# Kernel tuning notes

Hardware: AMD Instinct MI355X
Metric: run time of the kernel (lower is better)

## Reference

```python
import jax, jax.numpy as jnp
import numpy as np

B, NNODE, FIN, FOUT = 64, 512, 64, 64

def setup_inputs() -> dict:
    key = jax.random.key(0)
    ks = jax.random.split(key, 8)
    stdW = 1.0 / np.sqrt(FIN)
    stdA = 1.0 / np.sqrt(FOUT)
    return {
        "X": jax.random.normal(ks[0], (B, NNODE, FIN), dtype=jnp.float32),
        "A": jax.random.uniform(ks[1], (B, NNODE, NNODE), dtype=jnp.float32),
        "N": jax.random.randint(ks[2], (B,), 1, NNODE + 1, dtype=jnp.int64),
        "W": jax.random.uniform(ks[3], (FIN, FOUT), jnp.float32, -stdW, stdW),
        "a": jax.random.uniform(ks[4], (FOUT, FOUT), jnp.float32, -stdA, stdA),
        "bias_W": jax.random.uniform(ks[5], (FOUT,), jnp.float32, -stdW, stdW),
        "bias_a": jax.random.uniform(ks[6], (NNODE,), jnp.float32, -1.0 / np.sqrt(NNODE), 1.0 / np.sqrt(NNODE)),
    }

def reference(X, A, N, W, a, bias_W, bias_a):
    # A_ = A + identity on the top-left n_atoms block (only diagonal entries)
    idx = jnp.arange(A.shape[1])
    diag_mask = (idx[None, :] < N[:, None]).astype(A.dtype)  # [B, n]
    A_ = A + jnp.einsum('bn,nm->bnm', diag_mask, jnp.eye(A.shape[1], dtype=A.dtype))
    # XW: [B, n, F_out]
    XW = jnp.einsum('bnc,cd->bnd', X, W)
    # buf[a,j,k] = sum_i a[i,j] * XW^T[a,j,k]  (einsum 'ij,ajk->ajk')
    col_sum = a.sum(axis=0)  # [F_out]
    XWT = jnp.swapaxes(XW, 1, 2)  # [B, F_out, n]
    buf = col_sum[None, :, None] * XWT
    Z = jnp.einsum('bif,bfk->bik', XW, buf) + bias_a  # [B, n, n] + [n] broadcast on last dim
    att = jnp.tanh(jnp.einsum('bij,bjk->bik', A_, Z))
    H = jnp.einsum('bij,bjd->bid', att, XW) + bias_W
    return H
```

## Files before the change

### kernel.cpp

```cpp
#include <hip/hip_runtime.h>

#define BB 64
#define NN 512
#define FD 64

typedef short bf16x8 __attribute__((ext_vector_type(8)));
typedef float f32x4 __attribute__((ext_vector_type(4)));

__device__ __forceinline__ unsigned short f2bf(float f){
    unsigned u = __builtin_bit_cast(unsigned, f);
    u += 0x7fffu + ((u >> 16) & 1u);
    return (unsigned short)(u >> 16);
}
__device__ __forceinline__ float bf2f(unsigned short h){
    unsigned u = ((unsigned)h) << 16;
    return __builtin_bit_cast(float, u);
}
__device__ __forceinline__ float fast_tanh(float x){
    float e = __expf(2.0f * x);
    return 1.0f - 2.0f * __builtin_amdgcn_rcpf(e + 1.0f);
}
__device__ __forceinline__ bf16x8 pack8(float4 a, float4 b){
    bf16x8 r;
    r[0]=(short)f2bf(a.x); r[1]=(short)f2bf(a.y); r[2]=(short)f2bf(a.z); r[3]=(short)f2bf(a.w);
    r[4]=(short)f2bf(b.x); r[5]=(short)f2bf(b.y); r[6]=(short)f2bf(b.z); r[7]=(short)f2bf(b.w);
    return r;
}

__global__ __launch_bounds__(256) void k_prep(const float* __restrict__ W,
                                              const float* __restrict__ a,
                                              float* __restrict__ colsum,
                                              unsigned short* __restrict__ Wt){
    __shared__ float Wl[64][68];
    __shared__ float cpart[4][64];
    int t = threadIdx.x;
    int d = t & 63, part = t >> 6;
    float s = 0.f;
    #pragma unroll
    for (int i = 0; i < 16; i++) s += a[(part*16 + i)*64 + d];
    cpart[part][d] = s;
    int r = t >> 2, c0 = (t & 3) * 16;
    {
        const float4* src = (const float4*)&W[r*64 + c0];
        #pragma unroll
        for (int q = 0; q < 4; q++) *(float4*)&Wl[r][c0 + q*4] = src[q];
    }
    __syncthreads();
    if (part == 0) colsum[d] = cpart[0][d] + cpart[1][d] + cpart[2][d] + cpart[3][d];
    #pragma unroll
    for (int q = 0; q < 4; q++){
        ushort4 o;
        #pragma unroll
        for (int jj = 0; jj < 4; jj++)
            ((unsigned short*)&o)[jj] = f2bf(Wl[c0 + q*4 + jj][r]);
        *(ushort4*)&Wt[r*64 + c0 + q*4] = o;
    }
}

#define XWH_BYTE(n, f)  ((unsigned)(n)*128u + (((((unsigned)(f) >> 3) ^ ((unsigned)(n) & 7u)) & 7u) << 4) + (((unsigned)(f) & 7u) << 1))
#define XWH_B128(n, f0) ((unsigned)(n)*128u + (((((unsigned)(f0) >> 3) ^ ((unsigned)(n) & 7u)) & 7u) << 4))

__global__ __launch_bounds__(512, 1) void k_fused(const float* __restrict__ X,
                                               const float* __restrict__ A,
                                               const unsigned short* __restrict__ Wt,
                                               const float* __restrict__ colsum,
                                               const int* __restrict__ Ni,
                                               const float* __restrict__ bias_a,
                                               const float* __restrict__ bias_W,
                                               float* __restrict__ H){
    __shared__ unsigned short XWtL[64][520];
    __shared__ unsigned short XWhL[512*64];
    __shared__ unsigned short Pl[8][16][72];
    __shared__ unsigned short Wtl[64][72];
    __shared__ float bl[512];
    __shared__ float csl[64];
    int t = threadIdx.x;
    int b = blockIdx.x, it2 = blockIdx.y;
    int lane = t & 63, w = t >> 6, l15 = lane & 15, quad = lane >> 4;
    int tl = w >> 2, st = w & 3;
    int i0 = (it2 + 4*tl) * 64;
    int Nb = (Ni[1] == 0) ? Ni[2*b] : Ni[b];
    const float* Xb = X + (size_t)b*NN*FD;
    const float* Arow = A + (size_t)(b*NN + i0 + st*16 + l15)*NN + quad*8;

    float4 xv[8][2];
    #pragma unroll
    for (int rt = 0; rt < 4; rt++)
        #pragma unroll
        for (int ks = 0; ks < 2; ks++){
            const float* p = &Xb[(w*64 + rt*16 + l15)*FD + ks*32 + quad*8];
            xv[rt*2 + ks][0] = *(const float4*)p;
            xv[rt*2 + ks][1] = *(const float4*)(p + 4);
        }
    float4 pa[4][2];
    #pragma unroll
    for (int s = 0; s < 4; s++){
        pa[s][0] = *(const float4*)&Arow[s*32];
        pa[s][1] = *(const float4*)&Arow[s*32 + 4];
    }
    *(uint4*)&Wtl[t >> 3][(t & 7)*8] = *(const uint4*)&Wt[(t >> 3)*64 + (t & 7)*8];
    bl[t] = bias_a[t];
    if (t < 64) csl[t] = colsum[t];
    __syncthreads();

    #pragma unroll
    for (int rt = 0; rt < 4; rt++){
        f32x4 c[4] = {{0,0,0,0},{0,0,0,0},{0,0,0,0},{0,0,0,0}};
        #pragma unroll
        for (int ks = 0; ks < 2; ks++){
            bf16x8 af = pack8(xv[rt*2 + ks][0], xv[rt*2 + ks][1]);
            #pragma unroll
            for (int nt = 0; nt < 4; nt++){
                bf16x8 bfr = *(const bf16x8*)&Wtl[nt*16 + l15][ks*32 + quad*8];
                c[nt] = __builtin_amdgcn_mfma_f32_16x16x32_bf16(af, bfr, c[nt], 0, 0, 0);
            }
        }
        #pragma unroll
        for (int nt = 0; nt < 4; nt++)
            #pragma unroll
            for (int rg = 0; rg < 4; rg++){
                unsigned short hb = f2bf(c[nt][rg]);
                int n = w*64 + rt*16 + quad*4 + rg, f = nt*16 + l15;
                *(unsigned short*)((char*)XWhL + XWH_BYTE(n, f)) = hb;
                XWtL[f][n] = hb;
            }
    }
    __syncthreads();

    f32x4 acc[4] = {{0,0,0,0},{0,0,0,0},{0,0,0,0},{0,0,0,0}};
    float rs = 0.f;
    #pragma unroll
    for (int s = 0; s < 16; s++){
        float4 v0 = pa[s & 3][0], v1 = pa[s & 3][1];
        if (s < 12){
            pa[s & 3][0] = *(const float4*)&Arow[(s + 4)*32];
            pa[s & 3][1] = *(const float4*)&Arow[(s + 4)*32 + 4];
        }
        rs += (v0.x + v0.y) + (v0.z + v0.w) + (v1.x + v1.y) + (v1.z + v1.w);
        bf16x8 af = pack8(v0, v1);
        #pragma unroll
        for (int nt = 0; nt < 4; nt++){
            bf16x8 bfr = *(const bf16x8*)&XWtL[nt*16 + l15][s*32 + quad*8];
            acc[nt] = __builtin_amdgcn_mfma_f32_16x16x32_bf16(af, bfr, acc[nt], 0, 0, 0);
        }
    }
    #pragma unroll
    for (int nt = 0; nt < 4; nt++)
        #pragma unroll
        for (int rg = 0; rg < 4; rg++){
            int i = i0 + st*16 + quad*4 + rg;
            if (i < Nb)
                acc[nt][rg] += bf2f(*(const unsigned short*)((const char*)XWhL + XWH_BYTE(i, nt*16 + l15)));
        }
    float rsum = rs;
    rsum += __shfl_xor(rsum, 16);
    rsum += __shfl_xor(rsum, 32);
    #pragma unroll
    for (int nt = 0; nt < 4; nt++){
        float cs = csl[nt*16 + l15];
        #pragma unroll
        for (int rg = 0; rg < 4; rg++)
            Pl[w][quad*4 + rg][nt*16 + l15] = f2bf(acc[nt][rg] * cs);
    }
    asm volatile("s_waitcnt lgkmcnt(0)" ::: "memory");
    __builtin_amdgcn_sched_barrier(0);
    bf16x8 maf[2];
    maf[0] = *(const bf16x8*)&Pl[w][l15][quad*8];
    maf[1] = *(const bf16x8*)&Pl[w][l15][32 + quad*8];
    float rs_r[4];
    #pragma unroll
    for (int rg = 0; rg < 4; rg++){
        int i = i0 + st*16 + quad*4 + rg;
        rs_r[rg] = __shfl(rsum, quad*4 + rg) + ((i < Nb) ? 1.f : 0.f);
    }

    f32x4 hacc[4] = {{0,0,0,0},{0,0,0,0},{0,0,0,0},{0,0,0,0}};
    #pragma unroll
    for (int jt = 0; jt < 8; jt++){
        #pragma unroll
        for (int nt = 0; nt < 4; nt++){
            int j = jt*64 + nt*16 + l15;
            float bv = bl[j];
            f32x4 arg = { rs_r[0]*bv, rs_r[1]*bv, rs_r[2]*bv, rs_r[3]*bv };
            #pragma unroll
            for (int ks = 0; ks < 2; ks++){
                bf16x8 bfr = *(const bf16x8*)((const char*)XWhL + XWH_B128(j, ks*32 + quad*8));
                arg = __builtin_amdgcn_mfma_f32_16x16x32_bf16(maf[ks], bfr, arg, 0, 0, 0);
            }
            #pragma unroll
            for (int rg = 0; rg < 4; rg++)
                Pl[w][quad*4 + rg][nt*16 + l15] = f2bf(fast_tanh(arg[rg]));
        }
        asm volatile("s_waitcnt lgkmcnt(0)" ::: "memory");
        __builtin_amdgcn_sched_barrier(0);
        #pragma unroll
        for (int ks = 0; ks < 2; ks++){
            bf16x8 paf = *(const bf16x8*)&Pl[w][l15][ks*32 + quad*8];
            #pragma unroll
            for (int dt = 0; dt < 4; dt++){
                bf16x8 bfr = *(const bf16x8*)&XWtL[dt*16 + l15][jt*64 + ks*32 + quad*8];
                hacc[dt] = __builtin_amdgcn_mfma_f32_16x16x32_bf16(paf, bfr, hacc[dt], 0, 0, 0);
            }
        }
    }
    #pragma unroll
    for (int dt = 0; dt < 4; dt++){
        float bw = bias_W[dt*16 + l15];
        #pragma unroll
        for (int rg = 0; rg < 4; rg++)
            H[(size_t)(b*NN + i0 + st*16 + quad*4 + rg)*FD + dt*16 + l15] = hacc[dt][rg] + bw;
    }
}

extern "C" void kernel_launch(void* const* d_in, const int* in_sizes, int n_in,
                              void* d_out, int out_size, void* d_ws, size_t ws_size,
                              hipStream_t stream){
    const float* X      = (const float*)d_in[0];
    const float* A      = (const float*)d_in[1];
    const int*   N      = (const int*)  d_in[2];
    const float* W      = (const float*)d_in[3];
    const float* a      = (const float*)d_in[4];
    const float* bias_W = (const float*)d_in[5];
    const float* bias_a = (const float*)d_in[6];
    float* H = (float*)d_out;
    char* ws = (char*)d_ws;

    unsigned short* Wt     = (unsigned short*)(ws);
    float*          colsum = (float*)(ws + 8192);

    k_prep <<<1, 256, 0, stream>>>(W, a, colsum, Wt);
    k_fused<<<dim3(BB, 4), 512, 0, stream>>>(X, A, Wt, colsum, N, bias_a, bias_W, H);
}
```

Measured before the change: 126.9 us.

## Swap MFMA operand order to produce transposed tiles and vectorize LDS/global stores

Swaps the A/B operands of the MFMA calls so that each lane's accumulator holds four consecutive columns of one row. This turns scalar 16-bit LDS stores and scalar output writes into packed uint2 and float4 stores. XW is computed twice, once normally and once transposed, and written into padded LDS arrays instead of the swizzled layout. W fragments now live in registers instead of LDS, and the A prefetch depth is doubled from 4 to 8 stages. The change trades extra MFMAs and register pressure for fewer LDS store instructions, fewer shuffles and wider global stores.

```diff
diff --git a/kernel.cpp b/kernel.cpp
--- a/kernel.cpp
+++ b/kernel.cpp
@@ -15,6 +15,9 @@
 __device__ __forceinline__ float bf2f(unsigned short h){
     unsigned u = ((unsigned)h) << 16;
     return __builtin_bit_cast(float, u);
+}
+__device__ __forceinline__ unsigned pkbf2(float a, float b){
+    return (unsigned)f2bf(a) | ((unsigned)f2bf(b) << 16);
 }
 __device__ __forceinline__ float fast_tanh(float x){
     float e = __expf(2.0f * x);
@@ -57,9 +60,6 @@
     }
 }
 
-#define XWH_BYTE(n, f)  ((unsigned)(n)*128u + (((((unsigned)(f) >> 3) ^ ((unsigned)(n) & 7u)) & 7u) << 4) + (((unsigned)(f) & 7u) << 1))
-#define XWH_B128(n, f0) ((unsigned)(n)*128u + (((((unsigned)(f0) >> 3) ^ ((unsigned)(n) & 7u)) & 7u) << 4))
-
 __global__ __launch_bounds__(512, 1) void k_fused(const float* __restrict__ X,
                                                const float* __restrict__ A,
                                                const unsigned short* __restrict__ Wt,
@@ -69,9 +69,8 @@
                                                const float* __restrict__ bias_W,
                                                float* __restrict__ H){
     __shared__ unsigned short XWtL[64][520];
-    __shared__ unsigned short XWhL[512*64];
+    __shared__ unsigned short XWhL[512][72];
     __shared__ unsigned short Pl[8][16][72];
-    __shared__ unsigned short Wtl[64][72];
     __shared__ float bl[512];
     __shared__ float csl[64];
     int t = threadIdx.x;
@@ -92,123 +91,125 @@
             xv[rt*2 + ks][0] = *(const float4*)p;
             xv[rt*2 + ks][1] = *(const float4*)(p + 4);
         }
-    float4 pa[4][2];
-    #pragma unroll
-    for (int s = 0; s < 4; s++){
+    bf16x8 wf[4][2];
+    #pragma unroll
+    for (int ft = 0; ft < 4; ft++)
+        #pragma unroll
+        for (int ks = 0; ks < 2; ks++)
+            wf[ft][ks] = *(const bf16x8*)&Wt[(ft*16 + l15)*64 + ks*32 + quad*8];
+    bl[t] = bias_a[t];
+    if (t < 64) csl[t] = colsum[t];
+
+    #pragma unroll
+    for (int rt = 0; rt < 4; rt++){
+        bf16x8 af0 = pack8(xv[rt*2][0],     xv[rt*2][1]);
+        bf16x8 af1 = pack8(xv[rt*2 + 1][0], xv[rt*2 + 1][1]);
+        f32x4 c[4]  = {{0,0,0,0},{0,0,0,0},{0,0,0,0},{0,0,0,0}};
+        f32x4 ct[4] = {{0,0,0,0},{0,0,0,0},{0,0,0,0},{0,0,0,0}};
+        #pragma unroll
+        for (int nt = 0; nt < 4; nt++){
+            c[nt]  = __builtin_amdgcn_mfma_f32_16x16x32_bf16(af0, wf[nt][0], c[nt], 0, 0, 0);
+            c[nt]  = __builtin_amdgcn_mfma_f32_16x16x32_bf16(af1, wf[nt][1], c[nt], 0, 0, 0);
+            ct[nt] = __builtin_amdgcn_mfma_f32_16x16x32_bf16(wf[nt][0], af0, ct[nt], 0, 0, 0);
+            ct[nt] = __builtin_amdgcn_mfma_f32_16x16x32_bf16(wf[nt][1], af1, ct[nt], 0, 0, 0);
+        }
+        int n0 = w*64 + rt*16;
+        #pragma unroll
+        for (int nt = 0; nt < 4; nt++){
+            uint2 pk = { pkbf2(c[nt][0], c[nt][1]), pkbf2(c[nt][2], c[nt][3]) };
+            *(uint2*)&XWtL[nt*16 + l15][n0 + quad*4] = pk;
+        }
+        #pragma unroll
+        for (int ft = 0; ft < 4; ft++){
+            uint2 pk = { pkbf2(ct[ft][0], ct[ft][1]), pkbf2(ct[ft][2], ct[ft][3]) };
+            *(uint2*)&XWhL[n0 + l15][ft*16 + quad*4] = pk;
+        }
+    }
+    float4 pa[8][2];
+    #pragma unroll
+    for (int s = 0; s < 8; s++){
         pa[s][0] = *(const float4*)&Arow[s*32];
         pa[s][1] = *(const float4*)&Arow[s*32 + 4];
     }
-    *(uint4*)&Wtl[t >> 3][(t & 7)*8] = *(const uint4*)&Wt[(t >> 3)*64 + (t & 7)*8];
-    bl[t] = bias_a[t];
-    if (t < 64) csl[t] = colsum[t];
-    __syncthreads();
-
-    #pragma unroll
-    for (int rt = 0; rt < 4; rt++){
-        f32x4 c[4] = {{0,0,0,0},{0,0,0,0},{0,0,0,0},{0,0,0,0}};
-        #pragma unroll
-        for (int ks = 0; ks < 2; ks++){
-            bf16x8 af = pack8(xv[rt*2 + ks][0], xv[rt*2 + ks][1]);
-            #pragma unroll
-            for (int nt = 0; nt < 4; nt++){
-                bf16x8 bfr = *(const bf16x8*)&Wtl[nt*16 + l15][ks*32 + quad*8];
-                c[nt] = __builtin_amdgcn_mfma_f32_16x16x32_bf16(af, bfr, c[nt], 0, 0, 0);
-            }
-        }
-        #pragma unroll
-        for (int nt = 0; nt < 4; nt++)
-            #pragma unroll
-            for (int rg = 0; rg < 4; rg++){
-                unsigned short hb = f2bf(c[nt][rg]);
-                int n = w*64 + rt*16 + quad*4 + rg, f = nt*16 + l15;
-                *(unsigned short*)((char*)XWhL + XWH_BYTE(n, f)) = hb;
-                XWtL[f][n] = hb;
-            }
-    }
     __syncthreads();
 
     f32x4 acc[4] = {{0,0,0,0},{0,0,0,0},{0,0,0,0},{0,0,0,0}};
     float rs = 0.f;
     #pragma unroll
     for (int s = 0; s < 16; s++){
-        float4 v0 = pa[s & 3][0], v1 = pa[s & 3][1];
-        if (s < 12){
-            pa[s & 3][0] = *(const float4*)&Arow[(s + 4)*32];
-            pa[s & 3][1] = *(const float4*)&Arow[(s + 4)*32 + 4];
+        float4 v0 = pa[s & 7][0], v1 = pa[s & 7][1];
+        if (s < 8){
+            pa[s & 7][0] = *(const float4*)&Arow[(s + 8)*32];
+            pa[s & 7][1] = *(const float4*)&Arow[(s + 8)*32 + 4];
         }
         rs += (v0.x + v0.y) + (v0.z + v0.w) + (v1.x + v1.y) + (v1.z + v1.w);
         bf16x8 af = pack8(v0, v1);
         #pragma unroll
         for (int nt = 0; nt < 4; nt++){
-            bf16x8 bfr = *(const bf16x8*)&XWtL[nt*16 + l15][s*32 + quad*8];
-            acc[nt] = __builtin_amdgcn_mfma_f32_16x16x32_bf16(af, bfr, acc[nt], 0, 0, 0);
-        }
-    }
-    #pragma unroll
-    for (int nt = 0; nt < 4; nt++)
-        #pragma unroll
-        for (int rg = 0; rg < 4; rg++){
-            int i = i0 + st*16 + quad*4 + rg;
-            if (i < Nb)
-                acc[nt][rg] += bf2f(*(const unsigned short*)((const char*)XWhL + XWH_BYTE(i, nt*16 + l15)));
-        }
+            bf16x8 xa = *(const bf16x8*)&XWtL[nt*16 + l15][s*32 + quad*8];
+            acc[nt] = __builtin_amdgcn_mfma_f32_16x16x32_bf16(xa, af, acc[nt], 0, 0, 0);
+        }
+    }
+    int irow = i0 + st*16 + l15;
+    bool dg = irow < Nb;
+    #pragma unroll
+    for (int nt = 0; nt < 4; nt++){
+        float4 cs4 = *(const float4*)&csl[nt*16 + quad*4];
+        ushort4 dh = *(const ushort4*)&XWhL[irow][nt*16 + quad*4];
+        float m0 = (acc[nt][0] + (dg ? bf2f(dh.x) : 0.f)) * cs4.x;
+        float m1 = (acc[nt][1] + (dg ? bf2f(dh.y) : 0.f)) * cs4.y;
+        float m2 = (acc[nt][2] + (dg ? bf2f(dh.z) : 0.f)) * cs4.z;
+        float m3 = (acc[nt][3] + (dg ? bf2f(dh.w) : 0.f)) * cs4.w;
+        uint2 pk = { pkbf2(m0, m1), pkbf2(m2, m3) };
+        *(uint2*)&Pl[w][l15][nt*16 + quad*4] = pk;
+    }
     float rsum = rs;
     rsum += __shfl_xor(rsum, 16);
     rsum += __shfl_xor(rsum, 32);
-    #pragma unroll
-    for (int nt = 0; nt < 4; nt++){
-        float cs = csl[nt*16 + l15];
-        #pragma unroll
-        for (int rg = 0; rg < 4; rg++)
-            Pl[w][quad*4 + rg][nt*16 + l15] = f2bf(acc[nt][rg] * cs);
-    }
+    float rsum_l = rsum + (dg ? 1.f : 0.f);
     asm volatile("s_waitcnt lgkmcnt(0)" ::: "memory");
     __builtin_amdgcn_sched_barrier(0);
     bf16x8 maf[2];
     maf[0] = *(const bf16x8*)&Pl[w][l15][quad*8];
     maf[1] = *(const bf16x8*)&Pl[w][l15][32 + quad*8];
-    float rs_r[4];
-    #pragma unroll
-    for (int rg = 0; rg < 4; rg++){
-        int i = i0 + st*16 + quad*4 + rg;
-        rs_r[rg] = __shfl(rsum, quad*4 + rg) + ((i < Nb) ? 1.f : 0.f);
-    }
 
     f32x4 hacc[4] = {{0,0,0,0},{0,0,0,0},{0,0,0,0},{0,0,0,0}};
+    float4 bwv[4];
+    #pragma unroll
+    for (int dt = 0; dt < 4; dt++) bwv[dt] = *(const float4*)&bias_W[dt*16 + quad*4];
     #pragma unroll
     for (int jt = 0; jt < 8; jt++){
         #pragma unroll
         for (int nt = 0; nt < 4; nt++){
-            int j = jt*64 + nt*16 + l15;
-            float bv = bl[j];
-            f32x4 arg = { rs_r[0]*bv, rs_r[1]*bv, rs_r[2]*bv, rs_r[3]*bv };
+            float4 blv = *(const float4*)&bl[jt*64 + nt*16 + quad*4];
+            f32x4 arg = { rsum_l*blv.x, rsum_l*blv.y, rsum_l*blv.z, rsum_l*blv.w };
             #pragma unroll
             for (int ks = 0; ks < 2; ks++){
-                bf16x8 bfr = *(const bf16x8*)((const char*)XWhL + XWH_B128(j, ks*32 + quad*8));
-                arg = __builtin_amdgcn_mfma_f32_16x16x32_bf16(maf[ks], bfr, arg, 0, 0, 0);
+                bf16x8 xh = *(const bf16x8*)&XWhL[jt*64 + nt*16 + l15][ks*32 + quad*8];
+                arg = __builtin_amdgcn_mfma_f32_16x16x32_bf16(xh, maf[ks], arg, 0, 0, 0);
             }
-            #pragma unroll
-            for (int rg = 0; rg < 4; rg++)
-                Pl[w][quad*4 + rg][nt*16 + l15] = f2bf(fast_tanh(arg[rg]));
+            uint2 pk = { pkbf2(fast_tanh(arg[0]), fast_tanh(arg[1])),
+                         pkbf2(fast_tanh(arg[2]), fast_tanh(arg[3])) };
+            *(uint2*)&Pl[w][l15][nt*16 + quad*4] = pk;
         }
         asm volatile("s_waitcnt lgkmcnt(0)" ::: "memory");
         __builtin_amdgcn_sched_barrier(0);
         #pragma unroll
         for (int ks = 0; ks < 2; ks++){
-            bf16x8 paf = *(const bf16x8*)&Pl[w][l15][ks*32 + quad*8];
+            bf16x8 pf = *(const bf16x8*)&Pl[w][l15][ks*32 + quad*8];
             #pragma unroll
             for (int dt = 0; dt < 4; dt++){
-                bf16x8 bfr = *(const bf16x8*)&XWtL[dt*16 + l15][jt*64 + ks*32 + quad*8];
-                hacc[dt] = __builtin_amdgcn_mfma_f32_16x16x32_bf16(paf, bfr, hacc[dt], 0, 0, 0);
+                bf16x8 xt = *(const bf16x8*)&XWtL[dt*16 + l15][jt*64 + ks*32 + quad*8];
+                hacc[dt] = __builtin_amdgcn_mfma_f32_16x16x32_bf16(xt, pf, hacc[dt], 0, 0, 0);
             }
         }
     }
+    float* Hrow = H + (size_t)(b*NN + irow)*FD;
     #pragma unroll
     for (int dt = 0; dt < 4; dt++){
-        float bw = bias_W[dt*16 + l15];
-        #pragma unroll
-        for (int rg = 0; rg < 4; rg++)
-            H[(size_t)(b*NN + i0 + st*16 + quad*4 + rg)*FD + dt*16 + l15] = hacc[dt][rg] + bw;
+        float4 hv = { hacc[dt][0] + bwv[dt].x, hacc[dt][1] + bwv[dt].y,
+                      hacc[dt][2] + bwv[dt].z, hacc[dt][3] + bwv[dt].w };
+        *(float4*)&Hrow[dt*16 + quad*4] = hv;
     }
 }
 
```

Result: faster. 124.3 us (-2.1%).
